# Kernel tuning notes

Measured on AMD Instinct MI355X. Metric: run time of the kernel, lower is better.

The kernel has to match this reference:

```python
import jax, jax.numpy as jnp
import numpy as np

B, S, D, H = 4, 2048, 1024, 16
DH = D // H  # head dim == module's 'scale'


def setup_inputs() -> dict:
    key = jax.random.key(0)
    ks = jax.random.split(key, 9)
    std = 1.0 / np.sqrt(D)
    return {
        "x": jax.random.normal(ks[0], (B, S, D), dtype=jnp.float32),
        "Wq": jax.random.normal(ks[1], (D, D), dtype=jnp.float32) * std,
        "bq": jax.random.normal(ks[2], (D,), dtype=jnp.float32) * std,
        "Wk": jax.random.normal(ks[3], (D, D), dtype=jnp.float32) * std,
        "bk": jax.random.normal(ks[4], (D,), dtype=jnp.float32) * std,
        "Wv": jax.random.normal(ks[5], (D, D), dtype=jnp.float32) * std,
        "bv": jax.random.normal(ks[6], (D,), dtype=jnp.float32) * std,
        "Wo": jax.random.normal(ks[7], (D, D), dtype=jnp.float32) * std,
        "bo": jax.random.normal(ks[8], (D,), dtype=jnp.float32) * std,
    }


def reference(x, Wq, bq, Wk, bk, Wv, bv, Wo, bo):
    b, s, d = x.shape
    # torch Linear: y = x @ W.T + b
    q = (x @ Wq.T + bq).reshape(b, s, H, DH).transpose(0, 2, 1, 3)  # [B,H,S,Dh]
    k = (x @ Wk.T + bk).reshape(b, s, H, DH).transpose(0, 2, 1, 3)
    v = (x @ Wv.T + bv).reshape(b, s, H, DH).transpose(0, 2, 1, 3)
    # scaled dot-product with causal mask (prefill: Tq == Tk, empty cache)
    scores = jnp.einsum("bhqd,bhkd->bhqk", q, k) / jnp.sqrt(
        jnp.asarray(DH, dtype=jnp.float32))
    causal = jnp.tril(jnp.ones((s, s), dtype=bool))  # [S,S]
    scores = jnp.where(causal, scores, jnp.asarray(-1e9, dtype=scores.dtype))
    attn = jax.nn.softmax(scores, axis=-1)
    out = jnp.einsum("bhqk,bhkd->bhqd", attn, v)  # [B,H,S,Dh]
    out = out.transpose(0, 2, 1, 3).reshape(b, s, d)
    return out @ Wo.T + bo
```

## Files before the change

kernel.cpp:

```cpp
#include <hip/hip_runtime.h>
#include <hip/hip_bf16.h>
#include <stdint.h>

#define NB 4
#define NS 2048
#define ND 1024
#define NH 16
#define NDH 64
#define NM (NB*NS)

typedef __attribute__((ext_vector_type(8))) short bf16x8;
typedef __attribute__((ext_vector_type(4))) float f32x4;
typedef __attribute__((ext_vector_type(16))) float f32x16;
typedef __attribute__((ext_vector_type(8))) unsigned short u16x8;

static __device__ __forceinline__ unsigned short f2bf(float f) {
  union { float f; unsigned u; } v; v.f = f;
  return (unsigned short)((v.u + 0x7FFFu + ((v.u >> 16) & 1u)) >> 16);
}

static __device__ __forceinline__ void gload_lds16(const void* g, void* l) {
  __builtin_amdgcn_global_load_lds(
      (__attribute__((address_space(1))) unsigned int*)(uintptr_t)g,
      (__attribute__((address_space(3))) unsigned int*)(uintptr_t)(size_t)(l),
      16, 0, 0);
}

static __device__ __forceinline__ unsigned cvtpk(float lo, float hi) {
  unsigned r;
  asm("v_cvt_pk_bf16_f32 %0, %1, %2" : "=v"(r) : "v"(lo), "v"(hi));
  return r;
}
static __device__ __forceinline__ void plswap(unsigned &a, unsigned &b) {
  asm("v_permlane32_swap_b32 %0, %1" : "+v"(a), "+v"(b));
}

__global__ void k_cvt_all(const float* __restrict__ x,
                          const float* __restrict__ s0, const float* __restrict__ s1,
                          const float* __restrict__ s2, const float* __restrict__ s3,
                          unsigned short* __restrict__ xd,
                          unsigned short* __restrict__ d0, unsigned short* __restrict__ d1,
                          unsigned short* __restrict__ d2, unsigned short* __restrict__ d3) {
  constexpr int NGX = NM*ND/8;
  constexpr int NGW = ND*ND/8;
  int i = blockIdx.x * blockDim.x + threadIdx.x;
  const float* src; unsigned short* dst; int j;
  if (i < NGX) { src = x; dst = xd; j = i; }
  else {
    const int k = i - NGX, m = k / NGW;
    j = k - m*NGW;
    src = m==0 ? s0 : (m==1 ? s1 : (m==2 ? s2 : s3));
    dst = m==0 ? d0 : (m==1 ? d1 : (m==2 ? d2 : d3));
  }
  const float4* s = (const float4*)src + (size_t)j * 2;
  float4 a = s[0], b = s[1];
  u16x8 o;
  o[0]=f2bf(a.x); o[1]=f2bf(a.y); o[2]=f2bf(a.z); o[3]=f2bf(a.w);
  o[4]=f2bf(b.x); o[5]=f2bf(b.y); o[6]=f2bf(b.z); o[7]=f2bf(b.w);
  *((u16x8*)dst + j) = o;
}

__global__ __launch_bounds__(256, 4)
void k_gemm_qkv(const unsigned short* __restrict__ A,
                const unsigned short* __restrict__ Wqp, const unsigned short* __restrict__ Wkp,
                const unsigned short* __restrict__ Wvp,
                const float* __restrict__ bqp, const float* __restrict__ bkp,
                const float* __restrict__ bvp,
                unsigned short* __restrict__ Qo, unsigned short* __restrict__ Ko,
                unsigned short* __restrict__ Vto, float qscale)
{
  constexpr int K = ND, BK = 32;
  __shared__ unsigned short Alds[2][128*BK];
  __shared__ unsigned short Blds[2][128*BK];
  const int bcf = blockIdx.x;
  const int mat = bcf >> 3, bc = bcf & 7;
  const unsigned short* W = mat==0 ? Wqp : (mat==1 ? Wkp : Wvp);
  const float* bias = mat==0 ? bqp : (mat==1 ? bkp : bvp);
  const float scale = mat==0 ? qscale : 1.0f;

  const int tid = threadIdx.x;
  const int wid = tid >> 6, lane = tid & 63;
  const int g = lane >> 4, lr = lane & 15;
  const int br = blockIdx.y;
  const int wr = (wid >> 1) << 6, wc = (wid & 1) << 6;

  f32x4 acc[4][4];
  #pragma unroll
  for (int m=0;m<4;m++)
    #pragma unroll
    for (int n=0;n<4;n++) acc[m][n] = f32x4{0.f,0.f,0.f,0.f};

  const unsigned short* Ab = A + (size_t)br*128*K;
  const unsigned short* Wb = W + (size_t)bc*128*K;
  const int r0 = tid >> 2, c0 = (tid & 3) * 8;
  const int r1 = (256 + tid) >> 2;

  auto stage = [&](int b, int k0) {
    gload_lds16(Ab + (size_t)r0*K + k0 + c0, &Alds[b][tid*8]);
    gload_lds16(Ab + (size_t)r1*K + k0 + c0, &Alds[b][(256+tid)*8]);
    gload_lds16(Wb + (size_t)r0*K + k0 + c0, &Blds[b][tid*8]);
    gload_lds16(Wb + (size_t)r1*K + k0 + c0, &Blds[b][(256+tid)*8]);
  };

  stage(0, 0);
  __syncthreads();
  int cur = 0;
  for (int k0 = 0; k0 < K; k0 += BK) {
    if (k0 + BK < K) stage(cur ^ 1, k0 + BK);
    bf16x8 af[4], bfr[4];
    #pragma unroll
    for (int m=0;m<4;m++) af[m]  = *(const bf16x8*)&Alds[cur][(wr + m*16 + lr)*BK + g*8];
    #pragma unroll
    for (int n=0;n<4;n++) bfr[n] = *(const bf16x8*)&Blds[cur][(wc + n*16 + lr)*BK + g*8];
    __builtin_amdgcn_s_setprio(1);
    #pragma unroll
    for (int m=0;m<4;m++)
      #pragma unroll
      for (int n=0;n<4;n++)
        acc[m][n] = __builtin_amdgcn_mfma_f32_16x16x32_bf16(af[m], bfr[n], acc[m][n], 0, 0, 0);
    __builtin_amdgcn_s_setprio(0);
    __syncthreads();
    cur ^= 1;
  }

  #pragma unroll
  for (int m=0;m<4;m++) {
    const int rbase = br*128 + wr + m*16 + g*4;
    #pragma unroll
    for (int n=0;n<4;n++) {
      const int col = bc*128 + wc + n*16 + lr;
      const float bv = bias[col];
      #pragma unroll
      for (int j=0;j<4;j++) {
        const int row = rbase + j;
        const float val = (acc[m][n][j] + bv) * scale;
        const int b = row >> 11, s = row & (NS-1), h = col >> 6, dh = col & 63;
        if (mat == 2)
          Vto[(((size_t)b*NH + h)*NDH + dh)*NS + s] = f2bf(val);
        else
          (mat==0 ? Qo : Ko)[(((size_t)b*NH + h)*NS + s)*NDH + dh] = f2bf(val);
      }
    }
  }
}

__global__ __launch_bounds__(256, 4)
void k_gemm_o(const unsigned short* __restrict__ A,
              const unsigned short* __restrict__ W,
              const float* __restrict__ bias,
              float* __restrict__ outp)
{
  constexpr int K = ND, BK = 32;
  __shared__ unsigned short Alds[128*BK];
  __shared__ unsigned short Blds[128*BK];
  const int tid = threadIdx.x;
  const int wid = tid >> 6, lane = tid & 63;
  const int g = lane >> 4, lr = lane & 15;
  const int bc = blockIdx.x, br = blockIdx.y;
  const int wr = (wid >> 1) << 6, wc = (wid & 1) << 6;

  f32x4 acc[4][4];
  #pragma unroll
  for (int m=0;m<4;m++)
    #pragma unroll
    for (int n=0;n<4;n++) acc[m][n] = f32x4{0.f,0.f,0.f,0.f};

  const unsigned short* Ab = A + (size_t)br*128*K;
  const unsigned short* Wb = W + (size_t)bc*128*K;
  const int r0 = tid >> 2, c0 = (tid & 3) * 8;
  const int r1 = (256 + tid) >> 2;

  for (int k0 = 0; k0 < K; k0 += BK) {
    gload_lds16(Ab + (size_t)r0*K + k0 + c0, &Alds[tid*8]);
    gload_lds16(Ab + (size_t)r1*K + k0 + c0, &Alds[(256+tid)*8]);
    gload_lds16(Wb + (size_t)r0*K + k0 + c0, &Blds[tid*8]);
    gload_lds16(Wb + (size_t)r1*K + k0 + c0, &Blds[(256+tid)*8]);
    __syncthreads();
    bf16x8 af[4], bfr[4];
    #pragma unroll
    for (int m=0;m<4;m++) af[m]  = *(const bf16x8*)&Alds[(wr + m*16 + lr)*BK + g*8];
    #pragma unroll
    for (int n=0;n<4;n++) bfr[n] = *(const bf16x8*)&Blds[(wc + n*16 + lr)*BK + g*8];
    #pragma unroll
    for (int m=0;m<4;m++)
      #pragma unroll
      for (int n=0;n<4;n++)
        acc[m][n] = __builtin_amdgcn_mfma_f32_16x16x32_bf16(af[m], bfr[n], acc[m][n], 0, 0, 0);
    __syncthreads();
  }

  #pragma unroll
  for (int m=0;m<4;m++) {
    const int rbase = br*128 + wr + m*16 + g*4;
    #pragma unroll
    for (int n=0;n<4;n++) {
      const int col = bc*128 + wc + n*16 + lr;
      const float bv = bias[col];
      #pragma unroll
      for (int j=0;j<4;j++)
        outp[(size_t)(rbase + j)*ND + col] = acc[m][n][j] + bv;
    }
  }
}

__global__ __launch_bounds__(256, 4)
void k_attn(const unsigned short* __restrict__ Qg,
            const unsigned short* __restrict__ Kg,
            const unsigned short* __restrict__ Vtg,
            unsigned short* __restrict__ Og)
{
  __shared__ unsigned short Klds[64*64];
  __shared__ unsigned short Vlds[64*64];
  __shared__ float scL[128];
  const int tid = threadIdx.x;
  const int wid = tid >> 6, lane = tid & 63;
  const int ql = lane & 31, hi = lane >> 5;
  const int bh = blockIdx.x;
  const int qt = (int)gridDim.y - 1 - (int)blockIdx.y;
  const int qbB = qt * 128;
  const int wq = qbB + wid * 32;

  const unsigned short* Qh  = Qg  + (size_t)bh*NS*NDH;
  const unsigned short* Kh  = Kg  + (size_t)bh*NS*NDH;
  const unsigned short* Vth = Vtg + (size_t)bh*NDH*NS;

  bf16x8 qf[4];
  #pragma unroll
  for (int ds=0; ds<4; ++ds)
    qf[ds] = *(const bf16x8*)(Qh + (size_t)(wq+ql)*NDH + ds*16 + hi*8);

  f32x16 acc0, acc1;
  #pragma unroll
  for (int r=0;r<16;++r) { acc0[r]=0.f; acc1[r]=0.f; }
  float lsum = 0.f;

  const int sr = tid >> 3, sc = tid & 7;
  const int swz = (sc ^ (sr & 7)) * 8;

  const int ntiles = 2*qt + 2;
  for (int kt = 0; kt < ntiles; ++kt) {
    const int kbase = kt << 6;
    #pragma unroll
    for (int c=0;c<2;c++)
      gload_lds16(Kh + (size_t)(kbase + c*32 + sr)*NDH + swz, &Klds[(c*256+tid)*8]);
    #pragma unroll
    for (int c=0;c<2;c++)
      gload_lds16(Vth + (size_t)(c*32 + sr)*NS + kbase + swz, &Vlds[(c*256+tid)*8]);
    __syncthreads();
    #pragma unroll
    for (int h32 = 0; h32 < 2; ++h32) {
      const int kb32 = kbase + h32*32;
      if (kb32 <= wq) {
        const int krow = h32*32 + ql;
        f32x16 st;
        #pragma unroll
        for (int r=0;r<16;++r) st[r] = 0.f;
        __builtin_amdgcn_s_setprio(1);
        #pragma unroll
        for (int ds=0; ds<4; ++ds) {
          bf16x8 kf = *(const bf16x8*)&Klds[krow*64 + (((ds*2+hi) ^ (krow&7))*8)];
          st = __builtin_amdgcn_mfma_f32_32x32x16_bf16(kf, qf[ds], st, 0,0,0);
        }
        __builtin_amdgcn_s_setprio(0);
        if (kb32 == wq) {
          #pragma unroll
          for (int r=0;r<16;++r) {
            const int koff = (r&3) + 8*(r>>2) + 4*hi;
            if (koff > ql) st[r] = -1e30f;
          }
        }
        float p[16]; float ls = 0.f;
        #pragma unroll
        for (int r=0;r<16;++r) { p[r] = __builtin_amdgcn_exp2f(st[r]); ls += p[r]; }
        lsum += ls;
        unsigned w0 = cvtpk(p[0],p[1]),  w1 = cvtpk(p[2],p[3]);
        unsigned w2 = cvtpk(p[4],p[5]),  w3 = cvtpk(p[6],p[7]);
        plswap(w0, w2); plswap(w1, w3);
        unsigned z0 = cvtpk(p[8],p[9]),  z1 = cvtpk(p[10],p[11]);
        unsigned z2 = cvtpk(p[12],p[13]),z3 = cvtpk(p[14],p[15]);
        plswap(z0, z2); plswap(z1, z3);
        union { unsigned u[4]; bf16x8 v; } pk0, pk1;
        pk0.u[0]=w0; pk0.u[1]=w1; pk0.u[2]=w2; pk0.u[3]=w3;
        pk1.u[0]=z0; pk1.u[1]=z1; pk1.u[2]=z2; pk1.u[3]=z3;
        __builtin_amdgcn_s_setprio(1);
        #pragma unroll
        for (int nt=0; nt<2; ++nt) {
          const int drow = nt*32 + ql;
          #pragma unroll
          for (int ksl=0; ksl<2; ++ksl) {
            const int slot = h32*4 + ksl*2 + hi;
            bf16x8 vf = *(const bf16x8*)&Vlds[drow*64 + ((slot ^ (drow&7))*8)];
            f32x16 &a = nt ? acc1 : acc0;
            a = __builtin_amdgcn_mfma_f32_32x32x16_bf16(ksl ? pk1.v : pk0.v, vf, a, 0,0,0);
          }
        }
        __builtin_amdgcn_s_setprio(0);
      }
    }
    __syncthreads();
  }

  const float l = lsum + __shfl_xor(lsum, 32, 64);
  scL[wid*32 + ql] = 1.0f / l;
  const int b = bh >> 4, h = bh & 15;
  #pragma unroll
  for (int rq=0; rq<4; ++rq) {
    f32x4 lv = *(const f32x4*)&scL[wid*32 + rq*8 + 4*hi];
    #pragma unroll
    for (int j=0;j<4;j++) {
      const float inv = lv[j];
      const int s = wq + rq*8 + 4*hi + j;
      unsigned short* orow = Og + ((size_t)b*NS + s)*ND + h*NDH;
      orow[ql]      = f2bf(acc0[rq*4+j] * inv);
      orow[32 + ql] = f2bf(acc1[rq*4+j] * inv);
    }
  }
}

extern "C" void kernel_launch(void* const* d_in, const int* in_sizes, int n_in,
                              void* d_out, int out_size, void* d_ws, size_t ws_size,
                              hipStream_t stream) {
  (void)in_sizes; (void)n_in; (void)out_size; (void)ws_size;
  const float* x  = (const float*)d_in[0];
  const float* Wq = (const float*)d_in[1];
  const float* bq = (const float*)d_in[2];
  const float* Wk = (const float*)d_in[3];
  const float* bk = (const float*)d_in[4];
  const float* Wv = (const float*)d_in[5];
  const float* bv = (const float*)d_in[6];
  const float* Wo = (const float*)d_in[7];
  const float* bo = (const float*)d_in[8];

  char* ws = (char*)d_ws;
  unsigned short* xb  = (unsigned short*)(ws + 0);
  unsigned short* Wqb = (unsigned short*)(ws + 16777216);
  unsigned short* Wkb = (unsigned short*)(ws + 18874368);
  unsigned short* Wvb = (unsigned short*)(ws + 20971520);
  unsigned short* Wob = (unsigned short*)(ws + 23068672);
  unsigned short* Qb  = (unsigned short*)(ws + 25165824);
  unsigned short* Kb  = (unsigned short*)(ws + 41943040);
  unsigned short* Vtb = (unsigned short*)(ws + 58720256);
  unsigned short* Ob  = (unsigned short*)(ws + 75497472);

  constexpr int CVT_BLOCKS = (NM*ND/8 + 4*ND*ND/8) / 256;
  k_cvt_all<<<dim3(CVT_BLOCKS), dim3(256), 0, stream>>>(
      x, Wq, Wk, Wv, Wo, xb, Wqb, Wkb, Wvb, Wob);

  const float qscale = 0.125f * 1.4426950408889634f;
  k_gemm_qkv<<<dim3(24, NM/128), dim3(256), 0, stream>>>(
      xb, Wqb, Wkb, Wvb, bq, bk, bv, Qb, Kb, Vtb, qscale);

  k_attn<<<dim3(NB*NH, NS/128), dim3(256), 0, stream>>>(Qb, Kb, Vtb, Ob);

  k_gemm_o<<<dim3(ND/128, NM/128), dim3(256), 0, stream>>>(Ob, Wob, bo, (float*)d_out);
}
```

Measured before the change: 179.7 us.

## Use BK=64 tiles with XOR-swizzled LDS layout in projection GEMMs

Both the QKV and output projection GEMMs move to a K-tile of 64 with an XOR swizzle on the global-to-LDS chunk placement and the matching fragment reads. The swizzle is meant to avoid LDS bank conflicts, and the deeper tile halves the number of barrier-separated iterations. The QKV kernel drops its double buffer, so loads are no longer overlapped with MFMA work. Staying at the same 32 KB of LDS keeps occupancy unchanged.

```diff
diff --git a/kernel.cpp b/kernel.cpp
--- a/kernel.cpp
+++ b/kernel.cpp
@@ -69,9 +69,9 @@
                 unsigned short* __restrict__ Qo, unsigned short* __restrict__ Ko,
                 unsigned short* __restrict__ Vto, float qscale)
 {
-  constexpr int K = ND, BK = 32;
-  __shared__ unsigned short Alds[2][128*BK];
-  __shared__ unsigned short Blds[2][128*BK];
+  constexpr int K = ND, BK = 64;
+  __shared__ unsigned short Alds[128*BK];
+  __shared__ unsigned short Blds[128*BK];
   const int bcf = blockIdx.x;
   const int mat = bcf >> 3, bc = bcf & 7;
   const unsigned short* W = mat==0 ? Wqp : (mat==1 ? Wkp : Wvp);
@@ -92,35 +92,45 @@
 
   const unsigned short* Ab = A + (size_t)br*128*K;
   const unsigned short* Wb = W + (size_t)bc*128*K;
-  const int r0 = tid >> 2, c0 = (tid & 3) * 8;
-  const int r1 = (256 + tid) >> 2;
-
-  auto stage = [&](int b, int k0) {
-    gload_lds16(Ab + (size_t)r0*K + k0 + c0, &Alds[b][tid*8]);
-    gload_lds16(Ab + (size_t)r1*K + k0 + c0, &Alds[b][(256+tid)*8]);
-    gload_lds16(Wb + (size_t)r0*K + k0 + c0, &Blds[b][tid*8]);
-    gload_lds16(Wb + (size_t)r1*K + k0 + c0, &Blds[b][(256+tid)*8]);
-  };
-
-  stage(0, 0);
-  __syncthreads();
-  int cur = 0;
+
+  int srow[4], gcol[4];
+  #pragma unroll
+  for (int l=0;l<4;l++) {
+    const int n = l*256 + tid;
+    srow[l] = n >> 3;
+    gcol[l] = ((n & 7) ^ (srow[l] & 7)) * 8;
+  }
+
   for (int k0 = 0; k0 < K; k0 += BK) {
-    if (k0 + BK < K) stage(cur ^ 1, k0 + BK);
-    bf16x8 af[4], bfr[4];
-    #pragma unroll
-    for (int m=0;m<4;m++) af[m]  = *(const bf16x8*)&Alds[cur][(wr + m*16 + lr)*BK + g*8];
-    #pragma unroll
-    for (int n=0;n<4;n++) bfr[n] = *(const bf16x8*)&Blds[cur][(wc + n*16 + lr)*BK + g*8];
-    __builtin_amdgcn_s_setprio(1);
-    #pragma unroll
-    for (int m=0;m<4;m++)
-      #pragma unroll
-      for (int n=0;n<4;n++)
-        acc[m][n] = __builtin_amdgcn_mfma_f32_16x16x32_bf16(af[m], bfr[n], acc[m][n], 0, 0, 0);
-    __builtin_amdgcn_s_setprio(0);
-    __syncthreads();
-    cur ^= 1;
+    #pragma unroll
+    for (int l=0;l<4;l++)
+      gload_lds16(Ab + (size_t)srow[l]*K + k0 + gcol[l], &Alds[(l*256+tid)*8]);
+    #pragma unroll
+    for (int l=0;l<4;l++)
+      gload_lds16(Wb + (size_t)srow[l]*K + k0 + gcol[l], &Blds[(l*256+tid)*8]);
+    __syncthreads();
+    #pragma unroll
+    for (int ks=0; ks<2; ++ks) {
+      bf16x8 af[4], bfr[4];
+      #pragma unroll
+      for (int m=0;m<4;m++) {
+        const int row = wr + m*16 + lr;
+        af[m] = *(const bf16x8*)&Alds[row*BK + (((ks*4+g) ^ (row&7))*8)];
+      }
+      #pragma unroll
+      for (int n=0;n<4;n++) {
+        const int row = wc + n*16 + lr;
+        bfr[n] = *(const bf16x8*)&Blds[row*BK + (((ks*4+g) ^ (row&7))*8)];
+      }
+      __builtin_amdgcn_s_setprio(1);
+      #pragma unroll
+      for (int m=0;m<4;m++)
+        #pragma unroll
+        for (int n=0;n<4;n++)
+          acc[m][n] = __builtin_amdgcn_mfma_f32_16x16x32_bf16(af[m], bfr[n], acc[m][n], 0, 0, 0);
+      __builtin_amdgcn_s_setprio(0);
+    }
+    __syncthreads();
   }
 
   #pragma unroll
@@ -150,7 +160,7 @@
               const float* __restrict__ bias,
               float* __restrict__ outp)
 {
-  constexpr int K = ND, BK = 32;
+  constexpr int K = ND, BK = 64;
   __shared__ unsigned short Alds[128*BK];
   __shared__ unsigned short Blds[128*BK];
   const int tid = threadIdx.x;
@@ -167,25 +177,44 @@
 
   const unsigned short* Ab = A + (size_t)br*128*K;
   const unsigned short* Wb = W + (size_t)bc*128*K;
-  const int r0 = tid >> 2, c0 = (tid & 3) * 8;
-  const int r1 = (256 + tid) >> 2;
+
+  int srow[4], gcol[4];
+  #pragma unroll
+  for (int l=0;l<4;l++) {
+    const int n = l*256 + tid;
+    srow[l] = n >> 3;
+    gcol[l] = ((n & 7) ^ (srow[l] & 7)) * 8;
+  }
 
   for (int k0 = 0; k0 < K; k0 += BK) {
-    gload_lds16(Ab + (size_t)r0*K + k0 + c0, &Alds[tid*8]);
-    gload_lds16(Ab + (size_t)r1*K + k0 + c0, &Alds[(256+tid)*8]);
-    gload_lds16(Wb + (size_t)r0*K + k0 + c0, &Blds[tid*8]);
-    gload_lds16(Wb + (size_t)r1*K + k0 + c0, &Blds[(256+tid)*8]);
-    __syncthreads();
-    bf16x8 af[4], bfr[4];
-    #pragma unroll
-    for (int m=0;m<4;m++) af[m]  = *(const bf16x8*)&Alds[(wr + m*16 + lr)*BK + g*8];
-    #pragma unroll
-    for (int n=0;n<4;n++) bfr[n] = *(const bf16x8*)&Blds[(wc + n*16 + lr)*BK + g*8];
-    #pragma unroll
-    for (int m=0;m<4;m++)
-      #pragma unroll
-      for (int n=0;n<4;n++)
-        acc[m][n] = __builtin_amdgcn_mfma_f32_16x16x32_bf16(af[m], bfr[n], acc[m][n], 0, 0, 0);
+    #pragma unroll
+    for (int l=0;l<4;l++)
+      gload_lds16(Ab + (size_t)srow[l]*K + k0 + gcol[l], &Alds[(l*256+tid)*8]);
+    #pragma unroll
+    for (int l=0;l<4;l++)
+      gload_lds16(Wb + (size_t)srow[l]*K + k0 + gcol[l], &Blds[(l*256+tid)*8]);
+    __syncthreads();
+    #pragma unroll
+    for (int ks=0; ks<2; ++ks) {
+      bf16x8 af[4], bfr[4];
+      #pragma unroll
+      for (int m=0;m<4;m++) {
+        const int row = wr + m*16 + lr;
+        af[m] = *(const bf16x8*)&Alds[row*BK + (((ks*4+g) ^ (row&7))*8)];
+      }
+      #pragma unroll
+      for (int n=0;n<4;n++) {
+        const int row = wc + n*16 + lr;
+        bfr[n] = *(const bf16x8*)&Blds[row*BK + (((ks*4+g) ^ (row&7))*8)];
+      }
+      __builtin_amdgcn_s_setprio(1);
+      #pragma unroll
+      for (int m=0;m<4;m++)
+        #pragma unroll
+        for (int n=0;n<4;n++)
+          acc[m][n] = __builtin_amdgcn_mfma_f32_16x16x32_bf16(af[m], bfr[n], acc[m][n], 0, 0, 0);
+      __builtin_amdgcn_s_setprio(0);
+    }
     __syncthreads();
   }
 
```

Result: faster. 163.2 us, median of 2 (-9.2%).

## Rewrite projection GEMM mainloop with BK=64, XOR-swizzled LDS and split-phase prefetch

Applied to the files above, without the earlier changes.

Both projection GEMMs now share one mainloop with a K tile of 64. LDS rows are XOR-swizzled to avoid bank conflicts, and A and B loads are staggered so each half of the MFMA work overlaps the next global-to-LDS transfer, with explicit waitcnt, barriers and raised priority. The output GEMM gains double buffering it lacked before. LDS per block grows to 64KB and launch bounds drop to 2 blocks per CU, trading occupancy for deeper pipelining; the hand-placed barriers and vmcnt counts must match exactly or results may race.

```diff
diff --git a/kernel.cpp b/kernel.cpp
--- a/kernel.cpp
+++ b/kernel.cpp
@@ -34,6 +34,8 @@
 static __device__ __forceinline__ void plswap(unsigned &a, unsigned &b) {
   asm("v_permlane32_swap_b32 %0, %1" : "+v"(a), "+v"(b));
 }
+
+#define CFENCE asm volatile("" ::: "memory")
 
 __global__ void k_cvt_all(const float* __restrict__ x,
                           const float* __restrict__ s0, const float* __restrict__ s1,
@@ -60,7 +62,104 @@
   *((u16x8*)dst + j) = o;
 }
 
-__global__ __launch_bounds__(256, 4)
+#define GEMM_BODY                                                              \
+  constexpr int K = ND, BK = 64, NT = K / BK;                                  \
+  __shared__ unsigned short Al[2][128*BK];                     \
+  __shared__ unsigned short Bl[2][128*BK];                                     \
+  const int tid = threadIdx.x;                                                 \
+  const int wid = tid >> 6, lane = tid & 63;                                   \
+  const int g = lane >> 4, lr = lane & 15;                                     \
+  const int wr = (wid >> 1) << 6, wc = (wid & 1) << 6;                         \
+  f32x4 acc[4][4];                                                             \
+  _Pragma("unroll")                                                            \
+  for (int m=0;m<4;m++)                                                        \
+    _Pragma("unroll")                                                          \
+    for (int n=0;n<4;n++) acc[m][n] = f32x4{0.f,0.f,0.f,0.f};                  \
+  int srow[4], gcol[4];                                                        \
+  _Pragma("unroll")                                                            \
+  for (int l=0;l<4;l++) {                                                      \
+    const int n = l*256 + tid;                                                 \
+    srow[l] = n >> 3;                                                          \
+    gcol[l] = ((n & 7) ^ (srow[l] & 7)) * 8;                                   \
+  }                                                                            \
+  auto stageA = [&](int buf, int t) {                                          \
+    _Pragma("unroll")                                                          \
+    for (int l=0;l<4;l++)                                                      \
+      gload_lds16(Ab + (size_t)srow[l]*K + t*BK + gcol[l], &Al[buf][(l*256+tid)*8]); \
+  };                                                                           \
+  auto stageB = [&](int buf, int t) {                                          \
+    _Pragma("unroll")                                                          \
+    for (int l=0;l<4;l++)                                                      \
+      gload_lds16(Wb + (size_t)srow[l]*K + t*BK + gcol[l], &Bl[buf][(l*256+tid)*8]); \
+  };                                                                           \
+                 \
+  stageA(0, 0); stageB(0, 0); stageB(1, 1);                                    \
+  asm volatile("s_waitcnt vmcnt(4)" ::: "memory");                             \
+  __builtin_amdgcn_s_barrier();                                                \
+  CFENCE;                                                                      \
+  for (int t = 0; t < NT; ++t) {                                               \
+    const int cur = t & 1;                                                     \
+    const int tA = (t+1 < NT) ? t+1 : NT-1;                                    \
+    const int tB = (t+2 < NT) ? t+2 : NT-1;                                    \
+      \
+    bf16x8 bfr[8], af0[4];                                                     \
+    _Pragma("unroll")                                                          \
+    for (int n=0;n<4;n++) {                                                    \
+      const int row = wc + n*16 + lr;                                          \
+      _Pragma("unroll")                                                        \
+      for (int kk=0;kk<2;kk++)                                                 \
+        bfr[n*2+kk] = *(const bf16x8*)&Bl[cur][row*BK + (((kk*4+g) ^ (row&7))*8)]; \
+    }                                                                          \
+    _Pragma("unroll")                                                          \
+    for (int mm=0;mm<2;mm++) {                                                 \
+      const int row = wr + mm*16 + lr;                                         \
+      _Pragma("unroll")                                                        \
+      for (int kk=0;kk<2;kk++)                                                 \
+        af0[mm*2+kk] = *(const bf16x8*)&Al[cur][row*BK + (((kk*4+g) ^ (row&7))*8)]; \
+    }                                                                          \
+    stageA(cur ^ 1, tA);                                                       \
+    __builtin_amdgcn_s_barrier();                                              \
+    asm volatile("s_waitcnt lgkmcnt(0)" ::: "memory");                         \
+    __builtin_amdgcn_sched_barrier(0);                                         \
+    __builtin_amdgcn_s_setprio(1);                                             \
+    _Pragma("unroll")                                                          \
+    for (int mm=0;mm<2;mm++)                                                   \
+      _Pragma("unroll")                                                        \
+      for (int n=0;n<4;n++)                                                    \
+        _Pragma("unroll")                                                      \
+        for (int kk=0;kk<2;kk++)                                               \
+          acc[mm][n] = __builtin_amdgcn_mfma_f32_16x16x32_bf16(af0[mm*2+kk], bfr[n*2+kk], acc[mm][n], 0,0,0); \
+    __builtin_amdgcn_s_setprio(0);                                             \
+    __builtin_amdgcn_s_barrier();                                              \
+    CFENCE;                                                                    \
+     \
+    bf16x8 af1[4];                                                             \
+    _Pragma("unroll")                                                          \
+    for (int mm=0;mm<2;mm++) {                                                 \
+      const int row = wr + (2+mm)*16 + lr;                                     \
+      _Pragma("unroll")                                                        \
+      for (int kk=0;kk<2;kk++)                                                 \
+        af1[mm*2+kk] = *(const bf16x8*)&Al[cur][row*BK + (((kk*4+g) ^ (row&7))*8)]; \
+    }                                                                          \
+    stageB(cur, tB);                                                           \
+    asm volatile("s_waitcnt vmcnt(4)" ::: "memory");                           \
+    __builtin_amdgcn_s_barrier();                                              \
+    asm volatile("s_waitcnt lgkmcnt(0)" ::: "memory");                         \
+    __builtin_amdgcn_sched_barrier(0);                                         \
+    __builtin_amdgcn_s_setprio(1);                                             \
+    _Pragma("unroll")                                                          \
+    for (int mm=0;mm<2;mm++)                                                   \
+      _Pragma("unroll")                                                        \
+      for (int n=0;n<4;n++)                                                    \
+        _Pragma("unroll")                                                      \
+        for (int kk=0;kk<2;kk++)                                               \
+          acc[2+mm][n] = __builtin_amdgcn_mfma_f32_16x16x32_bf16(af1[mm*2+kk], bfr[n*2+kk], acc[2+mm][n], 0,0,0); \
+    __builtin_amdgcn_s_setprio(0);                                             \
+    __builtin_amdgcn_s_barrier();                                              \
+    CFENCE;                                                                    \
+  }
+
+__global__ __launch_bounds__(256, 2)
 void k_gemm_qkv(const unsigned short* __restrict__ A,
                 const unsigned short* __restrict__ Wqp, const unsigned short* __restrict__ Wkp,
                 const unsigned short* __restrict__ Wvp,
@@ -69,59 +168,16 @@
                 unsigned short* __restrict__ Qo, unsigned short* __restrict__ Ko,
                 unsigned short* __restrict__ Vto, float qscale)
 {
-  constexpr int K = ND, BK = 32;
-  __shared__ unsigned short Alds[2][128*BK];
-  __shared__ unsigned short Blds[2][128*BK];
   const int bcf = blockIdx.x;
   const int mat = bcf >> 3, bc = bcf & 7;
   const unsigned short* W = mat==0 ? Wqp : (mat==1 ? Wkp : Wvp);
   const float* bias = mat==0 ? bqp : (mat==1 ? bkp : bvp);
   const float scale = mat==0 ? qscale : 1.0f;
-
-  const int tid = threadIdx.x;
-  const int wid = tid >> 6, lane = tid & 63;
-  const int g = lane >> 4, lr = lane & 15;
   const int br = blockIdx.y;
-  const int wr = (wid >> 1) << 6, wc = (wid & 1) << 6;
-
-  f32x4 acc[4][4];
-  #pragma unroll
-  for (int m=0;m<4;m++)
-    #pragma unroll
-    for (int n=0;n<4;n++) acc[m][n] = f32x4{0.f,0.f,0.f,0.f};
-
-  const unsigned short* Ab = A + (size_t)br*128*K;
-  const unsigned short* Wb = W + (size_t)bc*128*K;
-  const int r0 = tid >> 2, c0 = (tid & 3) * 8;
-  const int r1 = (256 + tid) >> 2;
-
-  auto stage = [&](int b, int k0) {
-    gload_lds16(Ab + (size_t)r0*K + k0 + c0, &Alds[b][tid*8]);
-    gload_lds16(Ab + (size_t)r1*K + k0 + c0, &Alds[b][(256+tid)*8]);
-    gload_lds16(Wb + (size_t)r0*K + k0 + c0, &Blds[b][tid*8]);
-    gload_lds16(Wb + (size_t)r1*K + k0 + c0, &Blds[b][(256+tid)*8]);
-  };
-
-  stage(0, 0);
-  __syncthreads();
-  int cur = 0;
-  for (int k0 = 0; k0 < K; k0 += BK) {
-    if (k0 + BK < K) stage(cur ^ 1, k0 + BK);
-    bf16x8 af[4], bfr[4];
-    #pragma unroll
-    for (int m=0;m<4;m++) af[m]  = *(const bf16x8*)&Alds[cur][(wr + m*16 + lr)*BK + g*8];
-    #pragma unroll
-    for (int n=0;n<4;n++) bfr[n] = *(const bf16x8*)&Blds[cur][(wc + n*16 + lr)*BK + g*8];
-    __builtin_amdgcn_s_setprio(1);
-    #pragma unroll
-    for (int m=0;m<4;m++)
-      #pragma unroll
-      for (int n=0;n<4;n++)
-        acc[m][n] = __builtin_amdgcn_mfma_f32_16x16x32_bf16(af[m], bfr[n], acc[m][n], 0, 0, 0);
-    __builtin_amdgcn_s_setprio(0);
-    __syncthreads();
-    cur ^= 1;
-  }
+  const unsigned short* Ab = A + (size_t)br*128*ND;
+  const unsigned short* Wb = W + (size_t)bc*128*ND;
+
+  GEMM_BODY
 
   #pragma unroll
   for (int m=0;m<4;m++) {
@@ -130,11 +186,14 @@
     for (int n=0;n<4;n++) {
       const int col = bc*128 + wc + n*16 + lr;
       const float bv = bias[col];
+      const int h = col >> 6;
+      const int dh = col & 63;
       #pragma unroll
       for (int j=0;j<4;j++) {
         const int row = rbase + j;
         const float val = (acc[m][n][j] + bv) * scale;
-        const int b = row >> 11, s = row & (NS-1), h = col >> 6, dh = col & 63;
+        const int b = row >> 11;
+        const int s = row & (NS-1);
         if (mat == 2)
           Vto[(((size_t)b*NH + h)*NDH + dh)*NS + s] = f2bf(val);
         else
@@ -144,50 +203,17 @@
   }
 }
 
-__global__ __launch_bounds__(256, 4)
+__global__ __launch_bounds__(256, 2)
 void k_gemm_o(const unsigned short* __restrict__ A,
               const unsigned short* __restrict__ W,
               const float* __restrict__ bias,
               float* __restrict__ outp)
 {
-  constexpr int K = ND, BK = 32;
-  __shared__ unsigned short Alds[128*BK];
-  __shared__ unsigned short Blds[128*BK];
-  const int tid = threadIdx.x;
-  const int wid = tid >> 6, lane = tid & 63;
-  const int g = lane >> 4, lr = lane & 15;
   const int bc = blockIdx.x, br = blockIdx.y;
-  const int wr = (wid >> 1) << 6, wc = (wid & 1) << 6;
-
-  f32x4 acc[4][4];
-  #pragma unroll
-  for (int m=0;m<4;m++)
-    #pragma unroll
-    for (int n=0;n<4;n++) acc[m][n] = f32x4{0.f,0.f,0.f,0.f};
-
-  const unsigned short* Ab = A + (size_t)br*128*K;
-  const unsigned short* Wb = W + (size_t)bc*128*K;
-  const int r0 = tid >> 2, c0 = (tid & 3) * 8;
-  const int r1 = (256 + tid) >> 2;
-
-  for (int k0 = 0; k0 < K; k0 += BK) {
-    gload_lds16(Ab + (size_t)r0*K + k0 + c0, &Alds[tid*8]);
-    gload_lds16(Ab + (size_t)r1*K + k0 + c0, &Alds[(256+tid)*8]);
-    gload_lds16(Wb + (size_t)r0*K + k0 + c0, &Blds[tid*8]);
-    gload_lds16(Wb + (size_t)r1*K + k0 + c0, &Blds[(256+tid)*8]);
-    __syncthreads();
-    bf16x8 af[4], bfr[4];
-    #pragma unroll
-    for (int m=0;m<4;m++) af[m]  = *(const bf16x8*)&Alds[(wr + m*16 + lr)*BK + g*8];
-    #pragma unroll
-    for (int n=0;n<4;n++) bfr[n] = *(const bf16x8*)&Blds[(wc + n*16 + lr)*BK + g*8];
-    #pragma unroll
-    for (int m=0;m<4;m++)
-      #pragma unroll
-      for (int n=0;n<4;n++)
-        acc[m][n] = __builtin_amdgcn_mfma_f32_16x16x32_bf16(af[m], bfr[n], acc[m][n], 0, 0, 0);
-    __syncthreads();
-  }
+  const unsigned short* Ab = A + (size_t)br*128*ND;
+  const unsigned short* Wb = W + (size_t)bc*128*ND;
+
+  GEMM_BODY
 
   #pragma unroll
   for (int m=0;m<4;m++) {
```

New measurement: 167.4 us. 6.9% less time.
